# Optimization experiments

Hardware: AMD Instinct MI355X
Metric: run time of the kernel (lower is better)

Reference implementation:

```python
import jax, jax.numpy as jnp
import numpy as np

# ---- graph / model config (matches init_kwargs) ----
N_FUNC, N_IN, N_OUT = 10000, 2000, 2000
C = 8          # hidden channels per function node (fix_hidden_channels=True)
K_FF = 16      # function->function in-degree
K_IF = 4       # out-edges per input node
LAYERS = 4     # shared ResBlock applied `layers` times
B = 64
EPS = 1e-5
N_NODES = N_FUNC + N_IN + N_OUT
H = N_FUNC * C


def _build_graph():
    """Homogeneous edge list ordered [f->f, in->f, f->out] like hetero2homo,
    plus COO indices of W1 (E x H) and W3 (H x E) per get_conv_indices."""
    rng = np.random.default_rng(0)
    ff_dst = np.repeat(np.arange(N_FUNC), K_FF)
    ff_src = rng.integers(0, N_FUNC, ff_dst.shape[0])
    if_src = np.repeat(np.arange(N_IN) + N_FUNC, K_IF)
    if_dst = rng.integers(0, N_FUNC, if_src.shape[0])
    fo_dst = np.arange(N_OUT) + N_FUNC + N_IN
    fo_src = rng.integers(0, N_FUNC, N_OUT)
    src = np.concatenate([ff_src, if_src, fo_src]).astype(np.int32)
    dst = np.concatenate([ff_dst, if_dst, fo_dst]).astype(np.int32)
    # W1: edge e (dst = function node j) -> hidden channels j*C + c
    e1 = np.nonzero(dst < N_FUNC)[0]
    w1_row = np.repeat(e1, C).astype(np.int32)
    w1_col = (np.repeat(dst[e1].astype(np.int64), C) * C + np.tile(np.arange(C), e1.shape[0])).astype(np.int32)
    # W3: hidden channel src*C + c -> edge e (src = function node)
    e3 = np.nonzero(src < N_FUNC)[0]
    w3_col = np.repeat(e3, C).astype(np.int32)
    w3_row = (np.repeat(src[e3].astype(np.int64), C) * C + np.tile(np.arange(C), e3.shape[0])).astype(np.int32)
    return src, dst, w1_row, w1_col, w3_row, w3_col


def setup_inputs() -> dict:
    src, dst, w1_row, w1_col, w3_row, w3_col = _build_graph()
    key = jax.random.key(0)
    k0, k1, k2 = jax.random.split(key, 3)
    s1 = 1.0 / np.sqrt(K_FF * C)   # fan-based scale for W1 values
    s3 = 1.0 / np.sqrt(C)          # fan-based scale for W3 values
    E = src.shape[0]
    return {
        "x": jax.random.normal(k0, (B, N_IN), jnp.float32),
        "w1_val": jax.random.normal(k1, (w1_row.shape[0],), jnp.float32) * s1,
        "b1": jnp.zeros((H,), jnp.float32),
        "w3_val": jax.random.normal(k2, (w3_row.shape[0],), jnp.float32) * s3,
        "b3": jnp.zeros((E,), jnp.float32),
        "gamma": jnp.ones((H,), jnp.float32),
        "beta": jnp.zeros((H,), jnp.float32),
        "edge_src": jnp.asarray(src),
        "edge_dst": jnp.asarray(dst),
        "w1_row": jnp.asarray(w1_row),
        "w1_col": jnp.asarray(w1_col),
        "w3_row": jnp.asarray(w3_row),
        "w3_col": jnp.asarray(w3_col),
    }


def _sparse_linear(xin, row, col, val, bias, out_dim):
    # out[b, j] = sum_{(i,j) in nz} W[i,j] * x[b,i] + bias[j]
    contrib = xin[:, row] * val                      # [B, nnz]
    out = jnp.zeros((xin.shape[0], out_dim), xin.dtype).at[:, col].add(contrib)
    return out + bias


def _group_layernorm(h, gamma, beta):
    # fix_hidden_channels=True => equal-size groups of C channels per function node
    g = h.reshape(h.shape[0], N_FUNC, C)
    mu = g.mean(-1, keepdims=True)
    var = g.var(-1, keepdims=True)
    g = (g - mu) * jax.lax.rsqrt(var + EPS)
    return g.reshape(h.shape[0], -1) * gamma + beta


def reference(x, w1_val, b1, w3_val, b3, gamma, beta,
              edge_src, edge_dst, w1_row, w1_col, w3_row, w3_col):
    E = edge_src.shape[0]
    # node values -> edge values (node2edge gathers source-node value per edge)
    x_node = jnp.zeros((x.shape[0], N_NODES), x.dtype).at[:, N_FUNC:N_FUNC + N_IN].set(x)
    xe = x_node[:, edge_src]                          # [B, E]

    def block(xe):  # ResBlock: lin1 -> GroupLayerNorm -> GELU -> lin3 -> +residual
        h = _sparse_linear(xe, w1_row, w1_col, w1_val, b1, H)
        h = _group_layernorm(h, gamma, beta)
        h = jax.nn.gelu(h, approximate=False)
        return _sparse_linear(h, w3_row, w3_col, w3_val, b3, E) + xe

    for _ in range(LAYERS):  # share_layers=True: same weights each layer
        xe = block(xe)
    xe = xe / LAYERS

    # edge2node: each output node has exactly one incoming edge (the last N_OUT edges)
    out_idx = edge_dst[-N_OUT:] - (N_FUNC + N_IN)
    out = jnp.zeros((xe.shape[0], N_OUT), xe.dtype).at[:, out_idx].set(xe[:, -N_OUT:])
    return out
```

## Files before the change

kernel.cpp:

```cpp
#include <hip/hip_runtime.h>

#define N_FUNC 10000
#define N_IN   2000
#define N_OUT  2000
#define CCH    8
#define K_FF   16
#define E_TOTAL 170000
#define E_FF    160000
#define E_W1    168000
#define E_IF    8000
#define BATCH   64
#define N_LAYERS 4
#define EPS_LN  1e-5f

#define SRC_CAP 64
#define IF_CAP  16

__device__ __forceinline__ float bf2f(unsigned short u) {
    unsigned int x = ((unsigned int)u) << 16;
    return __builtin_bit_cast(float, x);
}
__device__ __forceinline__ unsigned short f2bf(float f) {
    unsigned int x = __builtin_bit_cast(unsigned int, f);
    unsigned int r = x + 0x7FFFu + ((x >> 16) & 1u);
    return (unsigned short)(r >> 16);
}


__global__ void prep_zero_xt(int* __restrict__ src_cnt, int* __restrict__ if_cnt,
                             const float* __restrict__ x, float* __restrict__ xT) {
    int i = blockIdx.x * blockDim.x + threadIdx.x;
    if (i < N_FUNC) { src_cnt[i] = 0; if_cnt[i] = 0; }
    if (i < N_IN * BATCH) {
        int col = i >> 6, lane = i & 63;
        xT[col * BATCH + lane] = x[lane * N_IN + col];
    }
}


__global__ void fill_buckets(const int* __restrict__ src, const int* __restrict__ dst,
                             int* __restrict__ src_cnt, int* __restrict__ src_bkt,
                             int* __restrict__ if_cnt, int* __restrict__ if_bkt) {
    int i = blockIdx.x * blockDim.x + threadIdx.x;
    if (i < E_FF + N_OUT) {
        int e = (i < E_FF) ? i : (E_W1 + (i - E_FF));
        int s = src[e];
        int pos = atomicAdd(&src_cnt[s], 1);
        src_bkt[s * SRC_CAP + pos] = e;
    }
    if (i < E_IF) {
        int e = E_FF + i;
        int d = dst[e];
        int pos = atomicAdd(&if_cnt[d], 1);
        if_bkt[d * IF_CAP + pos] = e;
    }
}


__device__ __forceinline__ void compute_h(
        const unsigned short* __restrict__ xe_old, const float* __restrict__ xT,
        const float* __restrict__ w1, const float* __restrict__ b1,
        const float* __restrict__ gamma, const float* __restrict__ beta,
        const float* __restrict__ b3, const int* __restrict__ if_cnt,
        const int* __restrict__ if_bkt, int f, int lane, int layer, bool first,
        float* __restrict__ hreg) {
    float acc[CCH];
    #pragma unroll
    for (int c = 0; c < CCH; c++) acc[c] = b1[f * CCH + c];

    if (!first) {
        float xv[K_FF];
        #pragma unroll
        for (int k = 0; k < K_FF; k++) xv[k] = bf2f(xe_old[(f * K_FF + k) * BATCH + lane]);
        #pragma unroll
        for (int k = 0; k < K_FF; k++) {
            const float* wr = w1 + (size_t)(f * K_FF + k) * CCH;
            #pragma unroll
            for (int c = 0; c < CCH; c++) acc[c] += xv[k] * wr[c];
        }
    }
    int icnt = if_cnt[f];
    float lf = (float)layer;
    for (int j = 0; j < icnt; j++) {
        int e = if_bkt[f * IF_CAP + j];
        int ii = (e - E_FF) >> 2;
        float xv = xT[ii * BATCH + lane] + lf * b3[e];
        const float* wr = w1 + (size_t)e * CCH;
        #pragma unroll
        for (int c = 0; c < CCH; c++) acc[c] += xv * wr[c];
    }
    float mu = 0.f;
    #pragma unroll
    for (int c = 0; c < CCH; c++) mu += acc[c];
    mu *= 0.125f;
    float var = 0.f;
    #pragma unroll
    for (int c = 0; c < CCH; c++) { float d = acc[c] - mu; var += d * d; }
    var *= 0.125f;
    float rs = rsqrtf(var + EPS_LN);
    #pragma unroll
    for (int c = 0; c < CCH; c++) {
        float g = (acc[c] - mu) * rs * gamma[f * CCH + c] + beta[f * CCH + c];
        hreg[c] = 0.5f * g * (1.0f + erff(g * 0.70710678118654752f));
    }
}

template <int CH>
__device__ __forceinline__ void scat_chunk(
        const int* __restrict__ bkt, int j, bool first,
        const unsigned short* __restrict__ xe_old, unsigned short* __restrict__ xe_new,
        const float* __restrict__ w3, const float* __restrict__ b3,
        const float* __restrict__ hreg, int lane) {
    int e[CH];
    float r[CH];
    #pragma unroll
    for (int q = 0; q < CH; q++) e[q] = bkt[j + q];
    #pragma unroll
    for (int q = 0; q < CH; q++)
        r[q] = first ? 0.f : bf2f(xe_old[(size_t)e[q] * BATCH + lane]);
    #pragma unroll
    for (int q = 0; q < CH; q++) {
        int p = (e[q] < E_FF) ? e[q] : (e[q] - E_IF);
        const float* wr = w3 + (size_t)p * CCH;
        float a = b3[e[q]] + r[q];
        #pragma unroll
        for (int c = 0; c < CCH; c++) a += hreg[c] * wr[c];
        xe_new[(size_t)e[q] * BATCH + lane] = f2bf(a);
    }
}


template <bool FIRST>
__global__ __launch_bounds__(256, 4) void layer_fused(
        const unsigned short* __restrict__ xe_old, unsigned short* __restrict__ xe_new,
        const float* __restrict__ xT, const float* __restrict__ w1,
        const float* __restrict__ b1, const float* __restrict__ gamma,
        const float* __restrict__ beta, const float* __restrict__ w3,
        const float* __restrict__ b3, const int* __restrict__ if_cnt,
        const int* __restrict__ if_bkt, const int* __restrict__ src_cnt,
        const int* __restrict__ src_bkt, int layer) {
    int wid = (blockIdx.x * blockDim.x + threadIdx.x) >> 6;
    int lane = threadIdx.x & 63;
    int f = __builtin_amdgcn_readfirstlane(wid);
    if (f >= N_FUNC) return;

    float hreg[CCH];
    compute_h(xe_old, xT, w1, b1, gamma, beta, b3, if_cnt, if_bkt,
              f, lane, layer, FIRST, hreg);

    const int* bkt = src_bkt + f * SRC_CAP;
    int ocnt = src_cnt[f];
    int j = 0;
    for (; j + 16 <= ocnt; j += 16)
        scat_chunk<16>(bkt, j, FIRST, xe_old, xe_new, w3, b3, hreg, lane);
    for (; j + 8 <= ocnt; j += 8)
        scat_chunk<8>(bkt, j, FIRST, xe_old, xe_new, w3, b3, hreg, lane);
    for (; j + 4 <= ocnt; j += 4)
        scat_chunk<4>(bkt, j, FIRST, xe_old, xe_new, w3, b3, hreg, lane);
    for (; j + 2 <= ocnt; j += 2)
        scat_chunk<2>(bkt, j, FIRST, xe_old, xe_new, w3, b3, hreg, lane);
    for (; j < ocnt; j++)
        scat_chunk<1>(bkt, j, FIRST, xe_old, xe_new, w3, b3, hreg, lane);
}


__global__ __launch_bounds__(256, 4) void layer_last(
        const unsigned short* __restrict__ xe_old, const float* __restrict__ xT,
        const float* __restrict__ w1, const float* __restrict__ b1,
        const float* __restrict__ gamma, const float* __restrict__ beta,
        const float* __restrict__ w3, const float* __restrict__ b3,
        const int* __restrict__ if_cnt, const int* __restrict__ if_bkt,
        const int* __restrict__ edge_src, float* __restrict__ out) {
    int wid = (blockIdx.x * blockDim.x + threadIdx.x) >> 6;
    int lane = threadIdx.x & 63;
    int j = __builtin_amdgcn_readfirstlane(wid);
    if (j >= N_OUT) return;
    int e = E_W1 + j;
    int s = __builtin_amdgcn_readfirstlane(edge_src[e]);

    float hreg[CCH];
    compute_h(xe_old, xT, w1, b1, gamma, beta, b3, if_cnt, if_bkt,
              s, lane, N_LAYERS - 1, false, hreg);

    int p = e - E_IF;
    const float* wr = w3 + (size_t)p * CCH;
    float acc = bf2f(xe_old[(size_t)e * BATCH + lane]) + b3[e];
    #pragma unroll
    for (int c = 0; c < CCH; c++) acc += hreg[c] * wr[c];
    out[lane * N_OUT + j] = acc * (1.0f / N_LAYERS);
}


extern "C" void kernel_launch(void* const* d_in, const int* in_sizes, int n_in,
                              void* d_out, int out_size, void* d_ws, size_t ws_size,
                              hipStream_t stream) {
    const float* x      = (const float*)d_in[0];
    const float* w1_val = (const float*)d_in[1];
    const float* b1     = (const float*)d_in[2];
    const float* w3_val = (const float*)d_in[3];
    const float* b3     = (const float*)d_in[4];
    const float* gamma  = (const float*)d_in[5];
    const float* beta   = (const float*)d_in[6];
    const int* edge_src = (const int*)d_in[7];
    const int* edge_dst = (const int*)d_in[8];
    float* out = (float*)d_out;

    char* base = (char*)d_ws;
    size_t off = 0;
    auto alloc = [&](size_t bytes) -> void* {
        void* p = base + off;
        off += (bytes + 255) & ~(size_t)255;
        return p;
    };
    unsigned short* xeA = (unsigned short*)alloc((size_t)E_TOTAL * BATCH * 2);
    unsigned short* xeB = (unsigned short*)alloc((size_t)E_TOTAL * BATCH * 2);
    float* xT     = (float*)alloc((size_t)N_IN * BATCH * 4);
    int* src_cnt  = (int*)alloc(N_FUNC * 4);
    int* if_cnt   = (int*)alloc(N_FUNC * 4);
    int* src_bkt  = (int*)alloc((size_t)N_FUNC * SRC_CAP * 4);
    int* if_bkt   = (int*)alloc((size_t)N_FUNC * IF_CAP * 4);
    (void)ws_size; (void)in_sizes; (void)n_in; (void)out_size;

    prep_zero_xt<<<(N_IN * BATCH + 255) / 256, 256, 0, stream>>>(src_cnt, if_cnt, x, xT);
    fill_buckets<<<(E_FF + N_OUT + 255) / 256, 256, 0, stream>>>(
        edge_src, edge_dst, src_cnt, src_bkt, if_cnt, if_bkt);

    layer_fused<true><<<(N_FUNC * BATCH) / 256, 256, 0, stream>>>(
        xeA, xeB, xT, w1_val, b1, gamma, beta, w3_val, b3,
        if_cnt, if_bkt, src_cnt, src_bkt, 0);
    layer_fused<false><<<(N_FUNC * BATCH) / 256, 256, 0, stream>>>(
        xeB, xeA, xT, w1_val, b1, gamma, beta, w3_val, b3,
        if_cnt, if_bkt, src_cnt, src_bkt, 1);
    layer_fused<false><<<(N_FUNC * BATCH) / 256, 256, 0, stream>>>(
        xeA, xeB, xT, w1_val, b1, gamma, beta, w3_val, b3,
        if_cnt, if_bkt, src_cnt, src_bkt, 2);
    layer_last<<<(N_OUT * BATCH) / 256, 256, 0, stream>>>(
        xeB, xT, w1_val, b1, gamma, beta, w3_val, b3,
        if_cnt, if_bkt, edge_src, out);
}
```

Before: 190.2 us.

## Carry per-node hidden sums instead of per-edge values and gather with W3

Uses the linearity of lin3 to change the per-layer state. Instead of 170k×64 bf16 edge values, each layer keeps a running sum of GELU outputs per function node (10k×512 bf16). Edge values are rebuilt on the fly inside a pull-style gather through W3, which removes the source buckets, the atomic bucket fill and the scatter writes. The exact erf GELU is also swapped for a tanh/sigmoid-style approximation. This trades cheaper memory traffic and a simpler setup for redundant W3 dot products per incoming edge and a small approximation error in GELU.

Result: faster. 173.0 us (-9.0%).

```diff
diff --git a/kernel.cpp b/kernel.cpp
--- a/kernel.cpp
+++ b/kernel.cpp
@@ -12,75 +12,60 @@
 #define BATCH   64
 #define N_LAYERS 4
 #define EPS_LN  1e-5f
-
-#define SRC_CAP 64
 #define IF_CAP  16
-
-__device__ __forceinline__ float bf2f(unsigned short u) {
-    unsigned int x = ((unsigned int)u) << 16;
-    return __builtin_bit_cast(float, x);
-}
-__device__ __forceinline__ unsigned short f2bf(float f) {
-    unsigned int x = __builtin_bit_cast(unsigned int, f);
-    unsigned int r = x + 0x7FFFu + ((x >> 16) & 1u);
-    return (unsigned short)(r >> 16);
-}
-
-
-__global__ void prep_zero_xt(int* __restrict__ src_cnt, int* __restrict__ if_cnt,
-                             const float* __restrict__ x, float* __restrict__ xT) {
+#define HROW    (BATCH * CCH)
+
+__device__ __forceinline__ float bfu_lo(unsigned int u) {
+    return __builtin_bit_cast(float, u << 16);
+}
+__device__ __forceinline__ float bfu_hi(unsigned int u) {
+    return __builtin_bit_cast(float, u & 0xffff0000u);
+}
+__device__ __forceinline__ unsigned int bfpack2(float f0, float f1) {
+    unsigned int x0 = __builtin_bit_cast(unsigned int, f0);
+    unsigned int x1 = __builtin_bit_cast(unsigned int, f1);
+    unsigned int r0 = (x0 + 0x7fffu + ((x0 >> 16) & 1u)) >> 16;
+    unsigned int r1 = (x1 + 0x7fffu + ((x1 >> 16) & 1u)) & 0xffff0000u;
+    return r0 | r1;
+}
+
+__device__ __forceinline__ float fast_gelu(float x) {
+    float x2 = x * x;
+    float u  = x * __builtin_fmaf(0.044715f, x2, 1.0f);
+    float e  = exp2f(-2.3022080f * u);
+    return x * (1.0f / (1.0f + e));
+}
+
+
+__global__ void zero_cnt(int* __restrict__ if_cnt) {
     int i = blockIdx.x * blockDim.x + threadIdx.x;
-    if (i < N_FUNC) { src_cnt[i] = 0; if_cnt[i] = 0; }
-    if (i < N_IN * BATCH) {
-        int col = i >> 6, lane = i & 63;
-        xT[col * BATCH + lane] = x[lane * N_IN + col];
-    }
-}
-
-
-__global__ void fill_buckets(const int* __restrict__ src, const int* __restrict__ dst,
-                             int* __restrict__ src_cnt, int* __restrict__ src_bkt,
-                             int* __restrict__ if_cnt, int* __restrict__ if_bkt) {
+    if (i < N_FUNC) if_cnt[i] = 0;
+}
+
+
+__global__ void fill_prep(const int* __restrict__ dst, const float* __restrict__ x,
+                          int* __restrict__ if_cnt, int* __restrict__ if_bkt,
+                          float* __restrict__ xT) {
     int i = blockIdx.x * blockDim.x + threadIdx.x;
-    if (i < E_FF + N_OUT) {
-        int e = (i < E_FF) ? i : (E_W1 + (i - E_FF));
-        int s = src[e];
-        int pos = atomicAdd(&src_cnt[s], 1);
-        src_bkt[s * SRC_CAP + pos] = e;
-    }
     if (i < E_IF) {
         int e = E_FF + i;
         int d = dst[e];
         int pos = atomicAdd(&if_cnt[d], 1);
         if_bkt[d * IF_CAP + pos] = e;
     }
-}
-
-
-__device__ __forceinline__ void compute_h(
-        const unsigned short* __restrict__ xe_old, const float* __restrict__ xT,
-        const float* __restrict__ w1, const float* __restrict__ b1,
-        const float* __restrict__ gamma, const float* __restrict__ beta,
-        const float* __restrict__ b3, const int* __restrict__ if_cnt,
-        const int* __restrict__ if_bkt, int f, int lane, int layer, bool first,
-        float* __restrict__ hreg) {
-    float acc[CCH];
-    #pragma unroll
-    for (int c = 0; c < CCH; c++) acc[c] = b1[f * CCH + c];
-
-    if (!first) {
-        float xv[K_FF];
-        #pragma unroll
-        for (int k = 0; k < K_FF; k++) xv[k] = bf2f(xe_old[(f * K_FF + k) * BATCH + lane]);
-        #pragma unroll
-        for (int k = 0; k < K_FF; k++) {
-            const float* wr = w1 + (size_t)(f * K_FF + k) * CCH;
-            #pragma unroll
-            for (int c = 0; c < CCH; c++) acc[c] += xv[k] * wr[c];
-        }
-    }
+    if (i < N_IN * BATCH) {
+        int col = i >> 6, lane = i & 63;
+        xT[col * BATCH + lane] = x[lane * N_IN + col];
+    }
+}
+
+
+__device__ __forceinline__ void if_accum(
+        float* __restrict__ acc, const float* __restrict__ xT,
+        const float* __restrict__ w1, const float* __restrict__ b3,
+        const int* __restrict__ if_cnt, const int* __restrict__ if_bkt,
+        int f, int lane, float lf) {
     int icnt = if_cnt[f];
-    float lf = (float)layer;
     for (int j = 0; j < icnt; j++) {
         int e = if_bkt[f * IF_CAP + j];
         int ii = (e - E_FF) >> 2;
@@ -89,6 +74,11 @@
         #pragma unroll
         for (int c = 0; c < CCH; c++) acc[c] += xv * wr[c];
     }
+}
+
+__device__ __forceinline__ void ln_gelu(
+        const float* __restrict__ acc, const float* __restrict__ gamma,
+        const float* __restrict__ beta, int f, float* __restrict__ hreg) {
     float mu = 0.f;
     #pragma unroll
     for (int c = 0; c < CCH; c++) mu += acc[c];
@@ -101,93 +91,128 @@
     #pragma unroll
     for (int c = 0; c < CCH; c++) {
         float g = (acc[c] - mu) * rs * gamma[f * CCH + c] + beta[f * CCH + c];
-        hreg[c] = 0.5f * g * (1.0f + erff(g * 0.70710678118654752f));
-    }
-}
-
-template <int CH>
-__device__ __forceinline__ void scat_chunk(
-        const int* __restrict__ bkt, int j, bool first,
-        const unsigned short* __restrict__ xe_old, unsigned short* __restrict__ xe_new,
+        hreg[c] = fast_gelu(g);
+    }
+}
+
+__device__ __forceinline__ void compute_h_gather(
+        const unsigned short* __restrict__ Hold, const float* __restrict__ xT,
+        const float* __restrict__ w1, const float* __restrict__ b1,
+        const float* __restrict__ gamma, const float* __restrict__ beta,
         const float* __restrict__ w3, const float* __restrict__ b3,
-        const float* __restrict__ hreg, int lane) {
-    int e[CH];
-    float r[CH];
-    #pragma unroll
-    for (int q = 0; q < CH; q++) e[q] = bkt[j + q];
-    #pragma unroll
-    for (int q = 0; q < CH; q++)
-        r[q] = first ? 0.f : bf2f(xe_old[(size_t)e[q] * BATCH + lane]);
-    #pragma unroll
-    for (int q = 0; q < CH; q++) {
-        int p = (e[q] < E_FF) ? e[q] : (e[q] - E_IF);
-        const float* wr = w3 + (size_t)p * CCH;
-        float a = b3[e[q]] + r[q];
+        const int* __restrict__ esrc, const int* __restrict__ if_cnt,
+        const int* __restrict__ if_bkt, int f, int lane, float lf,
+        float* __restrict__ hreg) {
+    int srcs[K_FF];
+    #pragma unroll
+    for (int k = 0; k < K_FF; k++) srcs[k] = esrc[f * K_FF + k];
+    uint4 hrow[K_FF];
+    #pragma unroll
+    for (int k = 0; k < K_FF; k++)
+        hrow[k] = *(const uint4*)(Hold + (size_t)srcs[k] * HROW + lane * CCH);
+
+    float acc[CCH];
+    #pragma unroll
+    for (int c = 0; c < CCH; c++) acc[c] = b1[f * CCH + c];
+
+    #pragma unroll
+    for (int k = 0; k < K_FF; k++) {
+        int e = f * K_FF + k;
+        const float* w3r = w3 + (size_t)e * CCH;
+        const float* w1r = w1 + (size_t)e * CCH;
+        float hv[CCH];
+        hv[0] = bfu_lo(hrow[k].x); hv[1] = bfu_hi(hrow[k].x);
+        hv[2] = bfu_lo(hrow[k].y); hv[3] = bfu_hi(hrow[k].y);
+        hv[4] = bfu_lo(hrow[k].z); hv[5] = bfu_hi(hrow[k].z);
+        hv[6] = bfu_lo(hrow[k].w); hv[7] = bfu_hi(hrow[k].w);
+        float xv = lf * b3[e];
         #pragma unroll
-        for (int c = 0; c < CCH; c++) a += hreg[c] * wr[c];
-        xe_new[(size_t)e[q] * BATCH + lane] = f2bf(a);
-    }
-}
-
-
-template <bool FIRST>
-__global__ __launch_bounds__(256, 4) void layer_fused(
-        const unsigned short* __restrict__ xe_old, unsigned short* __restrict__ xe_new,
-        const float* __restrict__ xT, const float* __restrict__ w1,
-        const float* __restrict__ b1, const float* __restrict__ gamma,
-        const float* __restrict__ beta, const float* __restrict__ w3,
+        for (int c = 0; c < CCH; c++) xv += hv[c] * w3r[c];
+        #pragma unroll
+        for (int c = 0; c < CCH; c++) acc[c] += xv * w1r[c];
+    }
+    if_accum(acc, xT, w1, b3, if_cnt, if_bkt, f, lane, lf);
+    ln_gelu(acc, gamma, beta, f, hreg);
+}
+
+
+__global__ __launch_bounds__(256, 4) void block_first(
+        unsigned short* __restrict__ Hnew, const float* __restrict__ xT,
+        const float* __restrict__ w1, const float* __restrict__ b1,
+        const float* __restrict__ gamma, const float* __restrict__ beta,
         const float* __restrict__ b3, const int* __restrict__ if_cnt,
-        const int* __restrict__ if_bkt, const int* __restrict__ src_cnt,
-        const int* __restrict__ src_bkt, int layer) {
+        const int* __restrict__ if_bkt) {
     int wid = (blockIdx.x * blockDim.x + threadIdx.x) >> 6;
     int lane = threadIdx.x & 63;
     int f = __builtin_amdgcn_readfirstlane(wid);
     if (f >= N_FUNC) return;
-
-    float hreg[CCH];
-    compute_h(xe_old, xT, w1, b1, gamma, beta, b3, if_cnt, if_bkt,
-              f, lane, layer, FIRST, hreg);
-
-    const int* bkt = src_bkt + f * SRC_CAP;
-    int ocnt = src_cnt[f];
-    int j = 0;
-    for (; j + 16 <= ocnt; j += 16)
-        scat_chunk<16>(bkt, j, FIRST, xe_old, xe_new, w3, b3, hreg, lane);
-    for (; j + 8 <= ocnt; j += 8)
-        scat_chunk<8>(bkt, j, FIRST, xe_old, xe_new, w3, b3, hreg, lane);
-    for (; j + 4 <= ocnt; j += 4)
-        scat_chunk<4>(bkt, j, FIRST, xe_old, xe_new, w3, b3, hreg, lane);
-    for (; j + 2 <= ocnt; j += 2)
-        scat_chunk<2>(bkt, j, FIRST, xe_old, xe_new, w3, b3, hreg, lane);
-    for (; j < ocnt; j++)
-        scat_chunk<1>(bkt, j, FIRST, xe_old, xe_new, w3, b3, hreg, lane);
-}
-
-
-__global__ __launch_bounds__(256, 4) void layer_last(
-        const unsigned short* __restrict__ xe_old, const float* __restrict__ xT,
+    float acc[CCH];
+    #pragma unroll
+    for (int c = 0; c < CCH; c++) acc[c] = b1[f * CCH + c];
+    if_accum(acc, xT, w1, b3, if_cnt, if_bkt, f, lane, 0.0f);
+    float h[CCH];
+    ln_gelu(acc, gamma, beta, f, h);
+    uint4 o;
+    o.x = bfpack2(h[0], h[1]); o.y = bfpack2(h[2], h[3]);
+    o.z = bfpack2(h[4], h[5]); o.w = bfpack2(h[6], h[7]);
+    *(uint4*)(Hnew + (size_t)f * HROW + lane * CCH) = o;
+}
+
+
+__global__ __launch_bounds__(256, 4) void block_mid(
+        const unsigned short* __restrict__ Hold, unsigned short* __restrict__ Hnew,
+        const float* __restrict__ xT, const float* __restrict__ w1,
+        const float* __restrict__ b1, const float* __restrict__ gamma,
+        const float* __restrict__ beta, const float* __restrict__ w3,
+        const float* __restrict__ b3, const int* __restrict__ esrc,
+        const int* __restrict__ if_cnt, const int* __restrict__ if_bkt, float lf) {
+    int wid = (blockIdx.x * blockDim.x + threadIdx.x) >> 6;
+    int lane = threadIdx.x & 63;
+    int f = __builtin_amdgcn_readfirstlane(wid);
+    if (f >= N_FUNC) return;
+    float h[CCH];
+    compute_h_gather(Hold, xT, w1, b1, gamma, beta, w3, b3, esrc,
+                     if_cnt, if_bkt, f, lane, lf, h);
+    uint4 own = *(const uint4*)(Hold + (size_t)f * HROW + lane * CCH);
+    uint4 o;
+    o.x = bfpack2(bfu_lo(own.x) + h[0], bfu_hi(own.x) + h[1]);
+    o.y = bfpack2(bfu_lo(own.y) + h[2], bfu_hi(own.y) + h[3]);
+    o.z = bfpack2(bfu_lo(own.z) + h[4], bfu_hi(own.z) + h[5]);
+    o.w = bfpack2(bfu_lo(own.w) + h[6], bfu_hi(own.w) + h[7]);
+    *(uint4*)(Hnew + (size_t)f * HROW + lane * CCH) = o;
+}
+
+
+__global__ __launch_bounds__(256, 4) void block_out(
+        const unsigned short* __restrict__ Hold, const float* __restrict__ xT,
         const float* __restrict__ w1, const float* __restrict__ b1,
         const float* __restrict__ gamma, const float* __restrict__ beta,
         const float* __restrict__ w3, const float* __restrict__ b3,
-        const int* __restrict__ if_cnt, const int* __restrict__ if_bkt,
-        const int* __restrict__ edge_src, float* __restrict__ out) {
+        const int* __restrict__ esrc, const int* __restrict__ if_cnt,
+        const int* __restrict__ if_bkt, float* __restrict__ out) {
     int wid = (blockIdx.x * blockDim.x + threadIdx.x) >> 6;
     int lane = threadIdx.x & 63;
     int j = __builtin_amdgcn_readfirstlane(wid);
     if (j >= N_OUT) return;
     int e = E_W1 + j;
-    int s = __builtin_amdgcn_readfirstlane(edge_src[e]);
-
-    float hreg[CCH];
-    compute_h(xe_old, xT, w1, b1, gamma, beta, b3, if_cnt, if_bkt,
-              s, lane, N_LAYERS - 1, false, hreg);
+    int s = __builtin_amdgcn_readfirstlane(esrc[e]);
+
+    float h[CCH];
+    compute_h_gather(Hold, xT, w1, b1, gamma, beta, w3, b3, esrc,
+                     if_cnt, if_bkt, s, lane, 3.0f, h);
+    uint4 own = *(const uint4*)(Hold + (size_t)s * HROW + lane * CCH);
+    float Hfin[CCH];
+    Hfin[0] = bfu_lo(own.x) + h[0]; Hfin[1] = bfu_hi(own.x) + h[1];
+    Hfin[2] = bfu_lo(own.y) + h[2]; Hfin[3] = bfu_hi(own.y) + h[3];
+    Hfin[4] = bfu_lo(own.z) + h[4]; Hfin[5] = bfu_hi(own.z) + h[5];
+    Hfin[6] = bfu_lo(own.w) + h[6]; Hfin[7] = bfu_hi(own.w) + h[7];
 
     int p = e - E_IF;
-    const float* wr = w3 + (size_t)p * CCH;
-    float acc = bf2f(xe_old[(size_t)e * BATCH + lane]) + b3[e];
-    #pragma unroll
-    for (int c = 0; c < CCH; c++) acc += hreg[c] * wr[c];
-    out[lane * N_OUT + j] = acc * (1.0f / N_LAYERS);
+    const float* w3r = w3 + (size_t)p * CCH;
+    float acc = 0.f;
+    #pragma unroll
+    for (int c = 0; c < CCH; c++) acc += Hfin[c] * w3r[c];
+    out[lane * N_OUT + j] = b3[e] + 0.25f * acc;
 }
 
 
@@ -212,29 +237,26 @@
         off += (bytes + 255) & ~(size_t)255;
         return p;
     };
-    unsigned short* xeA = (unsigned short*)alloc((size_t)E_TOTAL * BATCH * 2);
-    unsigned short* xeB = (unsigned short*)alloc((size_t)E_TOTAL * BATCH * 2);
-    float* xT     = (float*)alloc((size_t)N_IN * BATCH * 4);
-    int* src_cnt  = (int*)alloc(N_FUNC * 4);
-    int* if_cnt   = (int*)alloc(N_FUNC * 4);
-    int* src_bkt  = (int*)alloc((size_t)N_FUNC * SRC_CAP * 4);
-    int* if_bkt   = (int*)alloc((size_t)N_FUNC * IF_CAP * 4);
+    unsigned short* HsumA = (unsigned short*)alloc((size_t)N_FUNC * HROW * 2);
+    unsigned short* HsumB = (unsigned short*)alloc((size_t)N_FUNC * HROW * 2);
+    float* xT    = (float*)alloc((size_t)N_IN * BATCH * 4);
+    int* if_cnt  = (int*)alloc(N_FUNC * 4);
+    int* if_bkt  = (int*)alloc((size_t)N_FUNC * IF_CAP * 4);
     (void)ws_size; (void)in_sizes; (void)n_in; (void)out_size;
 
-    prep_zero_xt<<<(N_IN * BATCH + 255) / 256, 256, 0, stream>>>(src_cnt, if_cnt, x, xT);
-    fill_buckets<<<(E_FF + N_OUT + 255) / 256, 256, 0, stream>>>(
-        edge_src, edge_dst, src_cnt, src_bkt, if_cnt, if_bkt);
-
-    layer_fused<true><<<(N_FUNC * BATCH) / 256, 256, 0, stream>>>(
-        xeA, xeB, xT, w1_val, b1, gamma, beta, w3_val, b3,
-        if_cnt, if_bkt, src_cnt, src_bkt, 0);
-    layer_fused<false><<<(N_FUNC * BATCH) / 256, 256, 0, stream>>>(
-        xeB, xeA, xT, w1_val, b1, gamma, beta, w3_val, b3,
-        if_cnt, if_bkt, src_cnt, src_bkt, 1);
-    layer_fused<false><<<(N_FUNC * BATCH) / 256, 256, 0, stream>>>(
-        xeA, xeB, xT, w1_val, b1, gamma, beta, w3_val, b3,
-        if_cnt, if_bkt, src_cnt, src_bkt, 2);
-    layer_last<<<(N_OUT * BATCH) / 256, 256, 0, stream>>>(
-        xeB, xT, w1_val, b1, gamma, beta, w3_val, b3,
-        if_cnt, if_bkt, edge_src, out);
-}
+    zero_cnt<<<(N_FUNC + 255) / 256, 256, 0, stream>>>(if_cnt);
+    fill_prep<<<(N_IN * BATCH + 255) / 256, 256, 0, stream>>>(
+        edge_dst, x, if_cnt, if_bkt, xT);
+
+    block_first<<<(N_FUNC * BATCH) / 256, 256, 0, stream>>>(
+        HsumA, xT, w1_val, b1, gamma, beta, b3, if_cnt, if_bkt);
+    block_mid<<<(N_FUNC * BATCH) / 256, 256, 0, stream>>>(
+        HsumA, HsumB, xT, w1_val, b1, gamma, beta, w3_val, b3,
+        edge_src, if_cnt, if_bkt, 1.0f);
+    block_mid<<<(N_FUNC * BATCH) / 256, 256, 0, stream>>>(
+        HsumB, HsumA, xT, w1_val, b1, gamma, beta, w3_val, b3,
+        edge_src, if_cnt, if_bkt, 2.0f);
+    block_out<<<(N_OUT * BATCH) / 256, 256, 0, stream>>>(
+        HsumA, xT, w1_val, b1, gamma, beta, w3_val, b3,
+        edge_src, if_cnt, if_bkt, out);
+}
```
